# Optimization experiments

Measured on AMD Instinct MI355X. Metric: run time of the kernel, lower is better.

Reference implementation:

```python
import jax, jax.numpy as jnp
import numpy as np

# Static pyramid shapes (H, W) per level; must match setup_inputs().
SPATIAL_SHAPES = [(128, 128), (64, 64), (32, 32), (16, 16)]
N, LQ, D_MODEL, M, L, P = 2, 21760, 256, 8, 4, 4
D_HEAD = D_MODEL // M
LEN_IN = sum(h * w for h, w in SPATIAL_SHAPES)


def _bilinear_sample(v, grid, H, W):
    """torch.grid_sample(mode=bilinear, padding=zeros, align_corners=False).
    v: [B, H, W, D], grid: [B, Q, P, 2] (x, y) in [-1, 1] -> [B, Q, P, D]."""
    gx = (grid[..., 0] + 1.0) * (W * 0.5) - 0.5
    gy = (grid[..., 1] + 1.0) * (H * 0.5) - 0.5
    x0 = jnp.floor(gx)
    y0 = jnp.floor(gy)
    wx1 = gx - x0
    wy1 = gy - y0
    b = jnp.arange(v.shape[0])[:, None, None]

    def gather(yi, xi):
        valid = (xi >= 0) & (xi <= W - 1) & (yi >= 0) & (yi <= H - 1)
        xc = jnp.clip(xi, 0, W - 1).astype(jnp.int32)
        yc = jnp.clip(yi, 0, H - 1).astype(jnp.int32)
        return v[b, yc, xc] * valid[..., None].astype(v.dtype)

    return (gather(y0, x0) * ((1 - wy1) * (1 - wx1))[..., None]
            + gather(y0, x0 + 1) * ((1 - wy1) * wx1)[..., None]
            + gather(y0 + 1, x0) * (wy1 * (1 - wx1))[..., None]
            + gather(y0 + 1, x0 + 1) * (wy1 * wx1)[..., None])


def setup_inputs() -> dict:
    key = jax.random.key(0)
    ks = jax.random.split(key, 12)
    s = 0.02
    return {
        "query": jax.random.normal(ks[0], (N, LQ, D_MODEL), jnp.float32),
        "reference_points": jax.random.uniform(ks[1], (N, LQ, L, 2), jnp.float32),
        "value": jax.random.normal(ks[2], (N, LEN_IN, D_MODEL), jnp.float32),
        "value_spatial_shapes": jnp.array(SPATIAL_SHAPES, jnp.int32),
        "W_val": jax.random.normal(ks[3], (D_MODEL, D_MODEL), jnp.float32) * s,
        "b_val": jnp.zeros((D_MODEL,), jnp.float32),
        "W_off": jax.random.normal(ks[4], (D_MODEL, M * L * P * 2), jnp.float32) * s,
        "b_off": jax.random.normal(ks[5], (M * L * P * 2,), jnp.float32) * s,
        "W_attn": jax.random.normal(ks[6], (D_MODEL, M * L * P), jnp.float32) * s,
        "b_attn": jnp.zeros((M * L * P,), jnp.float32),
        "W_out": jax.random.normal(ks[7], (D_MODEL, D_MODEL), jnp.float32) * s,
        "b_out": jnp.zeros((D_MODEL,), jnp.float32),
    }


def reference(query, reference_points, value, value_spatial_shapes,
              W_val, b_val, W_off, b_off, W_attn, b_attn, W_out, b_out):
    # value_spatial_shapes is treated as static (SPATIAL_SHAPES) for jit safety.
    v = (value @ W_val + b_val).reshape(N, LEN_IN, M, D_HEAD)
    off = (query @ W_off + b_off).reshape(N, LQ, M, L, P, 2)
    aw = jax.nn.softmax((query @ W_attn + b_attn).reshape(N, LQ, M, L * P), axis=-1)
    aw = aw.reshape(N, LQ, M, L, P)
    # normalizer stacks (W, H) -> x normalized by W, y by H
    norm = jnp.array([[w, h] for h, w in SPATIAL_SHAPES], dtype=query.dtype)
    loc = reference_points[:, :, None, :, None, :] + off / norm[None, None, None, :, None, :]
    grid = 2.0 * loc - 1.0  # [N, LQ, M, L, P, 2]

    out = jnp.zeros((N * M, LQ, D_HEAD), query.dtype)
    start = 0
    for lid, (H, W) in enumerate(SPATIAL_SHAPES):
        vl = v[:, start:start + H * W].reshape(N, H, W, M, D_HEAD)
        vl = vl.transpose(0, 3, 1, 2, 4).reshape(N * M, H, W, D_HEAD)
        gl = grid[:, :, :, lid].transpose(0, 2, 1, 3, 4).reshape(N * M, LQ, P, 2)
        sl = _bilinear_sample(vl, gl, H, W)  # [N*M, LQ, P, D]
        wl = aw[:, :, :, lid].transpose(0, 2, 1, 3).reshape(N * M, LQ, P)
        out = out + jnp.einsum('bqpd,bqp->bqd', sl, wl)
        start += H * W

    out = out.reshape(N, M, LQ, D_HEAD).transpose(0, 2, 1, 3).reshape(N, LQ, D_MODEL)
    return out @ W_out + b_out
```

## Files before the change

### kernel.cpp

```cpp
#include <hip/hip_runtime.h>

typedef __attribute__((ext_vector_type(8))) short short8;
typedef __attribute__((ext_vector_type(4))) float floatx4;

#define N_    2
#define LQ_   21760
#define D_    256
#define M_    8
#define L_    4
#define P_    4
#define DH_   32
#define LEN_  21760
#define BQ    16

__constant__ int c_start[4] = {0, 16384, 20480, 21504};
__constant__ int c_HW[4]    = {128, 64, 32, 16};

#define WT_BYTE_OFF 22282240u

__device__ __forceinline__ unsigned short f2bf(float f) {
  unsigned int u = __builtin_bit_cast(unsigned int, f);
  u += 0x7fffu + ((u >> 16) & 1u);
  return (unsigned short)(u >> 16);
}
__device__ __forceinline__ float bf2f(unsigned short s) {
  return __builtin_bit_cast(float, ((unsigned int)s) << 16);
}

__global__ __launch_bounds__(256) void prep_kernel(
    const float* __restrict__ Woff, const float* __restrict__ Watt,
    const float* __restrict__ Wout, const float* __restrict__ Wv,
    unsigned short* __restrict__ wt) {
  const int b = blockIdx.x, t = threadIdx.x;
  const float* src; int ncols, n; unsigned short* dst;
  if (b < 256)      { src = Woff; ncols = 256; n = b;       dst = wt + 0      + n * 256; }
  else if (b < 384) { src = Watt; ncols = 128; n = b - 256; dst = wt + 65536  + n * 256; }
  else if (b < 640) { src = Wout; ncols = 256; n = b - 384; dst = wt + 98304  + n * 256; }
  else              { src = Wv;   ncols = 256; n = b - 640; dst = wt + 163840 + n * 256; }
  dst[t] = f2bf(src[(size_t)t * ncols + n]);
}

__global__ __launch_bounds__(256, 2) void vproj_kernel(
    const float* __restrict__ value, const unsigned short* __restrict__ Wvt,
    const float* __restrict__ bv, unsigned short* __restrict__ vout) {
  __shared__ unsigned short vs[64][264];
  const int t = threadIdx.x;
  const int r0 = blockIdx.x * 64;
  {
    const int c2 = (t & 127) * 2;
    const int rb = t >> 7;
#pragma unroll
    for (int i = 0; i < 32; ++i) {
      int rr = rb + i * 2;
      float2 v = *(const float2*)(value + (size_t)(r0 + rr) * D_ + c2);
      *(unsigned int*)&vs[rr][c2] = (unsigned int)f2bf(v.x) | ((unsigned int)f2bf(v.y) << 16);
    }
  }
  __syncthreads();
  const int wave = t >> 6, lane = t & 63;
  const int arow = wave * 16 + (lane & 15);
  const int kg = (lane >> 4) * 8;
  floatx4 acc[16] = {};
  for (int kk = 0; kk < 8; ++kk) {
    const int k0 = kk * 32;
    short8 af = *(const short8*)&vs[arow][k0 + kg];
#pragma unroll
    for (int ct = 0; ct < 16; ++ct) {
      const int col = ct * 16 + (lane & 15);
      short8 bf = *(const short8*)(Wvt + col * 256 + k0 + kg);
      acc[ct] = __builtin_amdgcn_mfma_f32_16x16x32_bf16(af, bf, acc[ct], 0, 0, 0);
    }
  }
  const int n = (r0 >= LEN_) ? 1 : 0;
  const int pixbase = r0 - n * LEN_ + wave * 16 + ((lane >> 4) * 4);
#pragma unroll
  for (int ct = 0; ct < 16; ++ct) {
    const int gc = ct * 16 + (lane & 15);
    const int m = gc >> 5, d = gc & 31;
    const float bb = bv[gc];
    unsigned short* ob = vout + ((size_t)(n * M_ + m) * LEN_) * DH_ + d;
#pragma unroll
    for (int j = 0; j < 4; ++j)
      ob[(size_t)(pixbase + j) * DH_] = f2bf(acc[ct][j] + bb);
  }
}

__global__ __launch_bounds__(256, 5) void msda_kernel(
    const float* __restrict__ query, const float* __restrict__ refp,
    const unsigned short* __restrict__ wt,
    const float* __restrict__ boff, const float* __restrict__ batt,
    const float* __restrict__ bout,
    const unsigned short* __restrict__ vproj, float* __restrict__ out) {
  __shared__ unsigned short qs[BQ][264];
  __shared__ unsigned short offb[BQ][256];
  __shared__ float awb[BQ][128];
  __shared__ short idxs[2][128][4];
  __shared__ float wls[2][128][4];

  const int t = threadIdx.x;
  const int qg0 = blockIdx.x * BQ;
  const int n = qg0 / LQ_;

  {
    const int c2 = (t & 127) * 2;
    const int rb = t >> 7;
#pragma unroll
    for (int i = 0; i < 8; ++i) {
      int rr = rb + i * 2;
      float2 v = *(const float2*)(query + (size_t)(qg0 + rr) * D_ + c2);
      *(unsigned int*)&qs[rr][c2] = (unsigned int)f2bf(v.x) | ((unsigned int)f2bf(v.y) << 16);
    }
  }
  __syncthreads();

  const int wave = t >> 6, lane = t & 63;
  const int arow = lane & 15;
  const int kg = (lane >> 4) * 8;
  const int row0 = (lane >> 4) * 4;

  {
    floatx4 acc[6] = {};
    for (int kk = 0; kk < 8; ++kk) {
      const int k0 = kk * 32;
      short8 af = *(const short8*)&qs[arow][k0 + kg];
#pragma unroll
      for (int i = 0; i < 6; ++i) {
        const int col = wave * 96 + i * 16 + (lane & 15);
        const unsigned short* bp = (col < 256) ? (wt + col * 256)
                                               : (wt + 65536 + (col - 256) * 256);
        short8 bf = *(const short8*)(bp + k0 + kg);
        acc[i] = __builtin_amdgcn_mfma_f32_16x16x32_bf16(af, bf, acc[i], 0, 0, 0);
      }
    }
#pragma unroll
    for (int i = 0; i < 6; ++i) {
      const int col = wave * 96 + i * 16 + (lane & 15);
      if (col < 256) {
        const float bb = boff[col];
#pragma unroll
        for (int j = 0; j < 4; ++j) offb[row0 + j][col] = f2bf(acc[i][j] + bb);
      } else {
        const float bb = batt[col - 256];
#pragma unroll
        for (int j = 0; j < 4; ++j) awb[row0 + j][col - 256] = acc[i][j] + bb;
      }
    }
  }
  __syncthreads();

  if (t < 128) {
    const int q = t >> 3, m = t & 7;
    float v[16]; float mx = -1e30f;
#pragma unroll
    for (int s = 0; s < 16; ++s) { v[s] = awb[q][m * 16 + s]; mx = fmaxf(mx, v[s]); }
    float sum = 0.f;
#pragma unroll
    for (int s = 0; s < 16; ++s) { v[s] = __expf(v[s] - mx); sum += v[s]; }
    const float inv = 1.f / sum;
#pragma unroll
    for (int s = 0; s < 16; ++s) awb[q][m * 16 + s] = v[s] * inv;
  }
  __syncthreads();

  const int m_g = t >> 5;
  const int g = t & 31;
  const int p8 = g >> 3;
  const int d4 = (g & 7) * 4;
  const unsigned short* vbase = vproj + ((size_t)(n * M_ + m_g) * LEN_) * DH_ + d4;

  for (int q = 0; q < BQ; ++q) {
    const int slot = q & 1;
    if (t < 128) {
      const int l = (t >> 2) & 3;
      const int Wl = c_HW[l];
      const int st = c_start[l];
      const float rx = refp[(((size_t)(qg0 + q)) * L_ + l) * 2 + 0];
      const float ry = refp[(((size_t)(qg0 + q)) * L_ + l) * 2 + 1];
      const float gx = rx * (float)Wl + bf2f(offb[q][2 * t])     - 0.5f;
      const float gy = ry * (float)Wl + bf2f(offb[q][2 * t + 1]) - 0.5f;
      const float fx0 = floorf(gx), fy0 = floorf(gy);
      const int x0 = (int)fx0, y0 = (int)fy0;
      const float wx1 = gx - fx0, wy1 = gy - fy0;
      const float wx0 = 1.f - wx1, wy0 = 1.f - wy1;
      const float a = awb[q][t];
      const bool vx0 = (x0 >= 0) && (x0 < Wl);
      const bool vx1 = (x0 + 1 >= 0) && (x0 + 1 < Wl);
      const bool vy0 = (y0 >= 0) && (y0 < Wl);
      const bool vy1 = (y0 + 1 >= 0) && (y0 + 1 < Wl);
      idxs[slot][t][0] = (short)((vx0 && vy0) ? st + y0 * Wl + x0 : -1);
      idxs[slot][t][1] = (short)((vx1 && vy0) ? st + y0 * Wl + x0 + 1 : -1);
      idxs[slot][t][2] = (short)((vx0 && vy1) ? st + (y0 + 1) * Wl + x0 : -1);
      idxs[slot][t][3] = (short)((vx1 && vy1) ? st + (y0 + 1) * Wl + x0 + 1 : -1);
      wls[slot][t][0] = wy0 * wx0 * a;
      wls[slot][t][1] = wy0 * wx1 * a;
      wls[slot][t][2] = wy1 * wx0 * a;
      wls[slot][t][3] = wy1 * wx1 * a;
    }
    __syncthreads();

    float a0 = 0.f, a1 = 0.f, a2 = 0.f, a3 = 0.f;
    const int sidb = m_g * 16;
#pragma unroll
    for (int s = 0; s < 16; ++s) {
      const int ix = (int)idxs[slot][sidb + s][p8];
      const int ixc = (ix >= 0) ? ix : 0;
      const float wv = (ix >= 0) ? wls[slot][sidb + s][p8] : 0.f;
      const unsigned short* p = vbase + (size_t)ixc * DH_;
      const uint2 u = *(const uint2*)p;
      a0 += __builtin_bit_cast(float, u.x << 16) * wv;
      a1 += __builtin_bit_cast(float, u.x & 0xffff0000u) * wv;
      a2 += __builtin_bit_cast(float, u.y << 16) * wv;
      a3 += __builtin_bit_cast(float, u.y & 0xffff0000u) * wv;
    }
    a0 += __shfl_xor(a0, 8);  a1 += __shfl_xor(a1, 8);
    a2 += __shfl_xor(a2, 8);  a3 += __shfl_xor(a3, 8);
    a0 += __shfl_xor(a0, 16); a1 += __shfl_xor(a1, 16);
    a2 += __shfl_xor(a2, 16); a3 += __shfl_xor(a3, 16);
    if (g < 8) {
      unsigned int* mp = (unsigned int*)&qs[q][m_g * 32 + d4];
      mp[0] = (unsigned int)f2bf(a0) | ((unsigned int)f2bf(a1) << 16);
      mp[1] = (unsigned int)f2bf(a2) | ((unsigned int)f2bf(a3) << 16);
    }
  }
  __syncthreads();

  {
    floatx4 acc[4] = {};
    for (int kk = 0; kk < 8; ++kk) {
      const int k0 = kk * 32;
      short8 af = *(const short8*)&qs[arow][k0 + kg];
#pragma unroll
      for (int i = 0; i < 4; ++i) {
        const int col = wave * 64 + i * 16 + (lane & 15);
        short8 bf = *(const short8*)(wt + 98304 + col * 256 + k0 + kg);
        acc[i] = __builtin_amdgcn_mfma_f32_16x16x32_bf16(af, bf, acc[i], 0, 0, 0);
      }
    }
#pragma unroll
    for (int i = 0; i < 4; ++i) {
      const int col = wave * 64 + i * 16 + (lane & 15);
      const float bb = bout[col];
#pragma unroll
      for (int j = 0; j < 4; ++j)
        out[(size_t)(qg0 + row0 + j) * D_ + col] = acc[i][j] + bb;
    }
  }
}

extern "C" void kernel_launch(void* const* d_in, const int* in_sizes, int n_in,
                              void* d_out, int out_size, void* d_ws, size_t ws_size,
                              hipStream_t stream) {
  const float* query = (const float*)d_in[0];
  const float* refp  = (const float*)d_in[1];
  const float* value = (const float*)d_in[2];
  const float* Wv    = (const float*)d_in[4];
  const float* bv    = (const float*)d_in[5];
  const float* Woff  = (const float*)d_in[6];
  const float* boff  = (const float*)d_in[7];
  const float* Watt  = (const float*)d_in[8];
  const float* batt  = (const float*)d_in[9];
  const float* Wout  = (const float*)d_in[10];
  const float* bout  = (const float*)d_in[11];
  float* out = (float*)d_out;

  unsigned short* vproj = (unsigned short*)d_ws;
  unsigned short* wt    = (unsigned short*)((char*)d_ws + WT_BYTE_OFF);
  const unsigned short* Wvt = wt + 163840;

  dim3 blk(256);
  hipLaunchKernelGGL(prep_kernel, dim3(896), blk, 0, stream, Woff, Watt, Wout, Wv, wt);
  hipLaunchKernelGGL(vproj_kernel, dim3((N_ * LEN_) / 64), blk, 0, stream, value, Wvt, bv, vproj);
  hipLaunchKernelGGL(msda_kernel, dim3((N_ * LQ_) / BQ), blk, 0, stream,
                     query, refp, wt, boff, batt, bout, vproj, out);
}
```

Baseline: 265.9 us.

## Coalesce bilinear corner gathers per row and remap blocks across XCDs

```diff
diff --git a/kernel.cpp b/kernel.cpp
--- a/kernel.cpp
+++ b/kernel.cpp
@@ -94,11 +94,12 @@
   __shared__ unsigned short qs[BQ][264];
   __shared__ unsigned short offb[BQ][256];
   __shared__ float awb[BQ][128];
-  __shared__ short idxs[2][128][4];
-  __shared__ float wls[2][128][4];
+  __shared__ short idxs2[2][128];
+  __shared__ float wls2[2][128][4];
 
   const int t = threadIdx.x;
-  const int qg0 = blockIdx.x * BQ;
+  const int lb = (blockIdx.x & 7) * 340 + (blockIdx.x >> 3);
+  const int qg0 = lb * BQ;
   const int n = qg0 / LQ_;
 
   {
@@ -164,9 +165,13 @@
 
   const int m_g = t >> 5;
   const int g = t & 31;
-  const int p8 = g >> 3;
+  const bool rowhi = (g & 16) != 0;
+  const int wsel = (g >> 3) & 3;
+  const int inrow = (g & 15) * 8;
   const int d4 = (g & 7) * 4;
-  const unsigned short* vbase = vproj + ((size_t)(n * M_ + m_g) * LEN_) * DH_ + d4;
+  const char* vbyte = (const char*)vproj + (size_t)(n * M_ + m_g) * LEN_ * DH_ * 2;
+
+  constexpr int kHW[4] = {128, 64, 32, 16};
 
   for (int q = 0; q < BQ; ++q) {
     const int slot = q & 1;
@@ -187,14 +192,11 @@
       const bool vx1 = (x0 + 1 >= 0) && (x0 + 1 < Wl);
       const bool vy0 = (y0 >= 0) && (y0 < Wl);
       const bool vy1 = (y0 + 1 >= 0) && (y0 + 1 < Wl);
-      idxs[slot][t][0] = (short)((vx0 && vy0) ? st + y0 * Wl + x0 : -1);
-      idxs[slot][t][1] = (short)((vx1 && vy0) ? st + y0 * Wl + x0 + 1 : -1);
-      idxs[slot][t][2] = (short)((vx0 && vy1) ? st + (y0 + 1) * Wl + x0 : -1);
-      idxs[slot][t][3] = (short)((vx1 && vy1) ? st + (y0 + 1) * Wl + x0 + 1 : -1);
-      wls[slot][t][0] = wy0 * wx0 * a;
-      wls[slot][t][1] = wy0 * wx1 * a;
-      wls[slot][t][2] = wy1 * wx0 * a;
-      wls[slot][t][3] = wy1 * wx1 * a;
+      idxs2[slot][t] = (short)(st + y0 * Wl + x0);
+      wls2[slot][t][0] = (vy0 && vx0) ? wy0 * wx0 * a : 0.f;
+      wls2[slot][t][1] = (vy0 && vx1) ? wy0 * wx1 * a : 0.f;
+      wls2[slot][t][2] = (vy1 && vx0) ? wy1 * wx0 * a : 0.f;
+      wls2[slot][t][3] = (vy1 && vx1) ? wy1 * wx1 * a : 0.f;
     }
     __syncthreads();
 
@@ -202,11 +204,12 @@
     const int sidb = m_g * 16;
 #pragma unroll
     for (int s = 0; s < 16; ++s) {
-      const int ix = (int)idxs[slot][sidb + s][p8];
-      const int ixc = (ix >= 0) ? ix : 0;
-      const float wv = (ix >= 0) ? wls[slot][sidb + s][p8] : 0.f;
-      const unsigned short* p = vbase + (size_t)ixc * DH_;
-      const uint2 u = *(const uint2*)p;
+      const int Wl_c = kHW[(s >> 2) & 3];
+      const int rb = (int)idxs2[slot][sidb + s] + (rowhi ? Wl_c : 0);
+      const float wv = wls2[slot][sidb + s][wsel];
+      int ofs = rb * 64 + inrow;
+      ofs = (ofs > 0) ? ofs : 0;
+      const uint2 u = *(const uint2*)(vbyte + ofs);
       a0 += __builtin_bit_cast(float, u.x << 16) * wv;
       a1 += __builtin_bit_cast(float, u.x & 0xffff0000u) * wv;
       a2 += __builtin_bit_cast(float, u.y << 16) * wv;
@@ -221,8 +224,8 @@
       mp[0] = (unsigned int)f2bf(a0) | ((unsigned int)f2bf(a1) << 16);
       mp[1] = (unsigned int)f2bf(a2) | ((unsigned int)f2bf(a3) << 16);
     }
-  }
-  __syncthreads();
+    __syncthreads();
+  }
 
   {
     floatx4 acc[4] = {};
```

After: 261.5 us. Within noise of the previous version (-1.7%).
